# Performance work log

Hardware: AMD Instinct MI355X
Metric: run time of the kernel (lower is better)

Reference implementation:

```python
import jax, jax.numpy as jnp
import numpy as np

NUM_ROUTING_ITER = 3

def _squash(x):
    # Faithful to torch x.norm(): GLOBAL Frobenius norm over the whole tensor.
    n2 = jnp.sum(x * x)
    return x * (jnp.sqrt(n2) / (1.0 + n2))

def setup_inputs() -> dict:
    key = jax.random.key(0)
    k1, k2 = jax.random.split(key)
    x = jax.random.normal(k1, (256, 1152, 8), dtype=jnp.float32)
    weight = jax.random.normal(k2, (10, 1152, 8, 16), dtype=jnp.float32)
    return {"x": x, "weight": weight}

def reference(x, weight):
    # priors: [NC, B, IC, 1, OC] from [1,B,IC,1,L] @ [NC,1,IC,L,OC]
    priors = jnp.einsum('bil,nilo->nbio', x, weight)[:, :, :, None, :]
    b = jnp.zeros_like(priors)
    v = None
    for _ in range(NUM_ROUTING_ITER):
        # legacy F.softmax with no dim on a 5D tensor -> dim=1 (batch dim)
        c = jax.nn.softmax(b, axis=1)
        s = jnp.sum(c * priors, axis=2, keepdims=True)  # [NC,B,1,1,OC]
        v = _squash(s)
        b = b + jnp.sum(priors * v, axis=-1, keepdims=True)
    return v
```

## Files before the change

### kernel.cpp

```cpp
#include <hip/hip_runtime.h>
#include <math.h>

#define NC    10
#define BATCH 256
#define IC    1152
#define LDIM  8
#define OC    16

#define NCH   96
#define CH    (IC/NCH)
#define NBLK  (NC*NCH)
#define NTHR  256
#define NTOT  (NC*BATCH*OC)
#define NRED  (NTOT/NTHR)

typedef float f32x2 __attribute__((ext_vector_type(2)));

__device__ __forceinline__ int xcd_swizzle(int bid, int nwg) {
    int cpx = nwg >> 3;
    return (bid & 7) * cpx + (bid >> 3);
}

__global__ __launch_bounds__(256) void k0_xT(const float* __restrict__ x,
                                             float* __restrict__ xT)
{
    int u = blockIdx.x * 256 + threadIdx.x;
    int i = u >> 9, r = u & 511, b = r >> 1, h = r & 1;
    reinterpret_cast<float4*>(xT)[u] =
        reinterpret_cast<const float4*>(x)[((size_t)b * IC + i) * 2 + h];
}

__global__ __launch_bounds__(256) void kA(
    const float* __restrict__ xT, const float* __restrict__ w,
    float* __restrict__ s_part)
{
    int wg = xcd_swizzle(blockIdx.x, NBLK);
    int n  = wg / NCH, ch = wg % NCH;
    int i0 = ch * CH;
    int t  = threadIdx.x;

    f32x2 sp2[8];
#pragma unroll
    for (int j = 0; j < 8; ++j) sp2[j] = (f32x2){0.f, 0.f};

    for (int ii = 0; ii < CH; ++ii) {
        int i = i0 + ii;
        const float4* xp = reinterpret_cast<const float4*>(xT)
                         + ((size_t)i * BATCH + t) * 2;
        float4 xa = xp[0], xb = xp[1];
        float xr[8] = {xa.x, xa.y, xa.z, xa.w, xb.x, xb.y, xb.z, xb.w};
        const f32x2* wp2 = reinterpret_cast<const f32x2*>(
            w + (size_t)__builtin_amdgcn_readfirstlane((n * IC + i) * (LDIM * OC)));
#pragma unroll
        for (int l = 0; l < LDIM; ++l) {
            f32x2 xl = {xr[l], xr[l]};
#pragma unroll
            for (int j = 0; j < 8; ++j)
                sp2[j] += wp2[l * 8 + j] * xl;
        }
    }
    float4* dst = reinterpret_cast<float4*>(s_part)
                + (((size_t)ch * NC + n) * BATCH + t) * 4;
    const float inv = 1.0f / 256.0f;
    dst[0] = make_float4(sp2[0].x*inv, sp2[0].y*inv, sp2[1].x*inv, sp2[1].y*inv);
    dst[1] = make_float4(sp2[2].x*inv, sp2[2].y*inv, sp2[3].x*inv, sp2[3].y*inv);
    dst[2] = make_float4(sp2[4].x*inv, sp2[4].y*inv, sp2[5].x*inv, sp2[5].y*inv);
    dst[3] = make_float4(sp2[6].x*inv, sp2[6].y*inv, sp2[7].x*inv, sp2[7].y*inv);
}

__global__ __launch_bounds__(256) void kR(const float* __restrict__ s_part,
                                          float* __restrict__ s,
                                          float* __restrict__ n2_part)
{
    int idx = blockIdx.x * 256 + threadIdx.x;
    float acc = 0.f;
    for (int c2 = 0; c2 < NCH; ++c2) acc += s_part[(size_t)c2 * NTOT + idx];
    s[idx] = acc;
    float q = acc * acc;
#pragma unroll
    for (int m = 32; m >= 1; m >>= 1) q += __shfl_xor(q, m, 64);
    __shared__ float r[4];
    int lane = threadIdx.x & 63, wid = threadIdx.x >> 6;
    if (lane == 0) r[wid] = q;
    __syncthreads();
    if (threadIdx.x == 0) n2_part[blockIdx.x] = r[0] + r[1] + r[2] + r[3];
}

template<bool FIRST>
__global__ __launch_bounds__(256) void kB(
    const float* __restrict__ xT, const float* __restrict__ w,
    const float* __restrict__ s, const float* __restrict__ n2_part,
    float* __restrict__ betaT, float* __restrict__ s_part)
{
    __shared__ float redA[2][4];
    __shared__ float redW[4];
    int t = threadIdx.x, lane = t & 63, wid = t >> 6;
    int wg = xcd_swizzle(blockIdx.x, NBLK);
    int n  = wg / NCH, ch = wg % NCH;
    int i0 = ch * CH;

    float q = (t < NRED) ? n2_part[t] : 0.f;
#pragma unroll
    for (int m = 32; m >= 1; m >>= 1) q += __shfl_xor(q, m, 64);
    if (lane == 0) redW[wid] = q;
    __syncthreads();
    float n2 = redW[0] + redW[1] + redW[2] + redW[3];
    float sc = sqrtf(n2) / (1.0f + n2);

    f32x2 v2[8];
    {
        const f32x2* svp = reinterpret_cast<const f32x2*>(s)
                         + ((size_t)n * BATCH + t) * 8;
        f32x2 scv = {sc, sc};
#pragma unroll
        for (int j = 0; j < 8; ++j) v2[j] = svp[j] * scv;
    }

    f32x2 sp2[8];
#pragma unroll
    for (int j = 0; j < 8; ++j) sp2[j] = (f32x2){0.f, 0.f};

    for (int ii = 0; ii < CH; ++ii) {
        int i = i0 + ii;
        const float4* xp = reinterpret_cast<const float4*>(xT)
                         + ((size_t)i * BATCH + t) * 2;
        float4 xa = xp[0], xb = xp[1];
        float xr[8] = {xa.x, xa.y, xa.z, xa.w, xb.x, xb.y, xb.z, xb.w};
        const f32x2* wp2 = reinterpret_cast<const f32x2*>(
            w + (size_t)__builtin_amdgcn_readfirstlane((n * IC + i) * (LDIM * OC)));

        f32x2 p2[8];
#pragma unroll
        for (int j = 0; j < 8; ++j) p2[j] = (f32x2){0.f, 0.f};
#pragma unroll
        for (int l = 0; l < LDIM; ++l) {
            f32x2 xl = {xr[l], xr[l]};
#pragma unroll
            for (int j = 0; j < 8; ++j)
                p2[j] += wp2[l * 8 + j] * xl;
        }

        f32x2 d2 = p2[0] * v2[0];
#pragma unroll
        for (int j = 1; j < 8; ++j) d2 += p2[j] * v2[j];
        float dot = d2.x + d2.y;

        size_t bidx = ((size_t)n * IC + i) * BATCH + t;
        float beta;
        if (FIRST) { beta = dot; betaT[bidx] = beta; }
        else       { beta = betaT[bidx] + dot; }

        float e = __expf(beta);
        float es = e;
#pragma unroll
        for (int m = 1; m < 64; m <<= 1) es += __shfl_xor(es, m, 64);
        if (lane == 0) redA[ii & 1][wid] = es;
        __syncthreads();
        float denom = redA[ii & 1][0] + redA[ii & 1][1]
                    + redA[ii & 1][2] + redA[ii & 1][3];
        float c = e * (1.0f / denom);
        f32x2 c2 = {c, c};
#pragma unroll
        for (int j = 0; j < 8; ++j) sp2[j] += c2 * p2[j];
    }

    float4* dst = reinterpret_cast<float4*>(s_part)
                + (((size_t)ch * NC + n) * BATCH + t) * 4;
    dst[0] = make_float4(sp2[0].x, sp2[0].y, sp2[1].x, sp2[1].y);
    dst[1] = make_float4(sp2[2].x, sp2[2].y, sp2[3].x, sp2[3].y);
    dst[2] = make_float4(sp2[4].x, sp2[4].y, sp2[5].x, sp2[5].y);
    dst[3] = make_float4(sp2[6].x, sp2[6].y, sp2[7].x, sp2[7].y);
}

__global__ __launch_bounds__(256) void k_out(const float* __restrict__ s,
                                             const float* __restrict__ n2_part,
                                             float* __restrict__ out)
{
    int t = threadIdx.x, lane = t & 63, wid = t >> 6;
    float q = (t < NRED) ? n2_part[t] : 0.f;
#pragma unroll
    for (int m = 32; m >= 1; m >>= 1) q += __shfl_xor(q, m, 64);
    __shared__ float r[4];
    if (lane == 0) r[wid] = q;
    __syncthreads();
    float n2 = r[0] + r[1] + r[2] + r[3];
    float sc = sqrtf(n2) / (1.0f + n2);
    int idx = blockIdx.x * 256 + t;
    out[idx] = s[idx] * sc;
}

extern "C" void kernel_launch(void* const* d_in, const int* in_sizes, int n_in,
                              void* d_out, int out_size, void* d_ws, size_t ws_size,
                              hipStream_t stream)
{
    const float* x = (const float*)d_in[0];
    const float* w = (const float*)d_in[1];
    float* out = (float*)d_out;
    float* ws  = (float*)d_ws;

    float* xT      = ws;
    float* betaT   = xT + (size_t)IC * BATCH * LDIM;
    float* s       = betaT + (size_t)NC * IC * BATCH;
    float* s_part  = s + (size_t)NC * BATCH * OC;
    float* n2_part = s_part + (size_t)NCH * NC * BATCH * OC;

    dim3 blk(256);

    k0_xT<<<2304, blk, 0, stream>>>(x, xT);
    kA<<<NBLK, blk, 0, stream>>>(xT, w, s_part);
    kR<<<NRED, blk, 0, stream>>>(s_part, s, n2_part);
    kB<true><<<NBLK, blk, 0, stream>>>(xT, w, s, n2_part, betaT, s_part);
    kR<<<NRED, blk, 0, stream>>>(s_part, s, n2_part);
    kB<false><<<NBLK, blk, 0, stream>>>(xT, w, s, n2_part, betaT, s_part);
    kR<<<NRED, blk, 0, stream>>>(s_part, s, n2_part);
    k_out<<<NRED, blk, 0, stream>>>(s, n2_part, out);
}
```

Before: 98.27 us.

## Double chunk count, split reduction across waves, and prefetch x in routing kernel

Doubles the number of input-capsule chunks so kA and kB launch twice as many workgroups, each handling fewer capsules. The partial-sum reduction kernel now splits the chunk loop across four waves per block with an LDS combine, producing 640 norm partials that a shared helper reduces. kB also software-prefetches the next capsule's x values to hide load latency behind the per-capsule barrier. In exchange, the partial-sum buffer doubles in size and the reduce reads more data.

```diff
diff --git a/kernel.cpp b/kernel.cpp
--- a/kernel.cpp
+++ b/kernel.cpp
@@ -7,18 +7,31 @@
 #define LDIM  8
 #define OC    16
 
-#define NCH   96
+#define NCH   192
 #define CH    (IC/NCH)
 #define NBLK  (NC*NCH)
 #define NTHR  256
 #define NTOT  (NC*BATCH*OC)
-#define NRED  (NTOT/NTHR)
+#define NRB   (NTOT/64)
+#define KPG   (NCH/4)
 
 typedef float f32x2 __attribute__((ext_vector_type(2)));
 
 __device__ __forceinline__ int xcd_swizzle(int bid, int nwg) {
     int cpx = nwg >> 3;
     return (bid & 7) * cpx + (bid >> 3);
+}
+
+__device__ __forceinline__ float n2_reduce(const float* __restrict__ n2_part,
+                                           float* redW, int t, int lane, int wid)
+{
+    float q = n2_part[t] + n2_part[t + 256];
+    if (t < 128) q += n2_part[t + 512];
+#pragma unroll
+    for (int m = 32; m >= 1; m >>= 1) q += __shfl_xor(q, m, 64);
+    if (lane == 0) redW[wid] = q;
+    __syncthreads();
+    return redW[0] + redW[1] + redW[2] + redW[3];
 }
 
 __global__ __launch_bounds__(256) void k0_xT(const float* __restrict__ x,
@@ -72,18 +85,22 @@
                                           float* __restrict__ s,
                                           float* __restrict__ n2_part)
 {
-    int idx = blockIdx.x * 256 + threadIdx.x;
+    __shared__ float lds[4][64];
+    int t = threadIdx.x, lane = t & 63, g = t >> 6;
+    int idx0 = blockIdx.x * 64;
     float acc = 0.f;
-    for (int c2 = 0; c2 < NCH; ++c2) acc += s_part[(size_t)c2 * NTOT + idx];
-    s[idx] = acc;
-    float q = acc * acc;
-#pragma unroll
-    for (int m = 32; m >= 1; m >>= 1) q += __shfl_xor(q, m, 64);
-    __shared__ float r[4];
-    int lane = threadIdx.x & 63, wid = threadIdx.x >> 6;
-    if (lane == 0) r[wid] = q;
+    for (int k = 0; k < KPG; ++k)
+        acc += s_part[(size_t)(g * KPG + k) * NTOT + idx0 + lane];
+    lds[g][lane] = acc;
     __syncthreads();
-    if (threadIdx.x == 0) n2_part[blockIdx.x] = r[0] + r[1] + r[2] + r[3];
+    if (t < 64) {
+        float sv = lds[0][t] + lds[1][t] + lds[2][t] + lds[3][t];
+        s[idx0 + t] = sv;
+        float q = sv * sv;
+#pragma unroll
+        for (int m = 32; m >= 1; m >>= 1) q += __shfl_xor(q, m, 64);
+        if (t == 0) n2_part[blockIdx.x] = q;
+    }
 }
 
 template<bool FIRST>
@@ -99,12 +116,7 @@
     int n  = wg / NCH, ch = wg % NCH;
     int i0 = ch * CH;
 
-    float q = (t < NRED) ? n2_part[t] : 0.f;
-#pragma unroll
-    for (int m = 32; m >= 1; m >>= 1) q += __shfl_xor(q, m, 64);
-    if (lane == 0) redW[wid] = q;
-    __syncthreads();
-    float n2 = redW[0] + redW[1] + redW[2] + redW[3];
+    float n2 = n2_reduce(n2_part, redW, t, lane, wid);
     float sc = sqrtf(n2) / (1.0f + n2);
 
     f32x2 v2[8];
@@ -120,11 +132,18 @@
 #pragma unroll
     for (int j = 0; j < 8; ++j) sp2[j] = (f32x2){0.f, 0.f};
 
+    const float4* xbase = reinterpret_cast<const float4*>(xT);
+    size_t xo = ((size_t)i0 * BATCH + t) * 2;
+    float4 xa = xbase[xo], xb = xbase[xo + 1];
+
     for (int ii = 0; ii < CH; ++ii) {
         int i = i0 + ii;
-        const float4* xp = reinterpret_cast<const float4*>(xT)
-                         + ((size_t)i * BATCH + t) * 2;
-        float4 xa = xp[0], xb = xp[1];
+        float4 na = xa, nb = xb;
+        if (ii + 1 < CH) {
+            size_t nx = ((size_t)(i + 1) * BATCH + t) * 2;
+            na = xbase[nx]; nb = xbase[nx + 1];
+        }
+
         float xr[8] = {xa.x, xa.y, xa.z, xa.w, xb.x, xb.y, xb.z, xb.w};
         const f32x2* wp2 = reinterpret_cast<const f32x2*>(
             w + (size_t)__builtin_amdgcn_readfirstlane((n * IC + i) * (LDIM * OC)));
@@ -162,6 +181,8 @@
         f32x2 c2 = {c, c};
 #pragma unroll
         for (int j = 0; j < 8; ++j) sp2[j] += c2 * p2[j];
+
+        xa = na; xb = nb;
     }
 
     float4* dst = reinterpret_cast<float4*>(s_part)
@@ -176,14 +197,9 @@
                                              const float* __restrict__ n2_part,
                                              float* __restrict__ out)
 {
+    __shared__ float redW[4];
     int t = threadIdx.x, lane = t & 63, wid = t >> 6;
-    float q = (t < NRED) ? n2_part[t] : 0.f;
-#pragma unroll
-    for (int m = 32; m >= 1; m >>= 1) q += __shfl_xor(q, m, 64);
-    __shared__ float r[4];
-    if (lane == 0) r[wid] = q;
-    __syncthreads();
-    float n2 = r[0] + r[1] + r[2] + r[3];
+    float n2 = n2_reduce(n2_part, redW, t, lane, wid);
     float sc = sqrtf(n2) / (1.0f + n2);
     int idx = blockIdx.x * 256 + t;
     out[idx] = s[idx] * sc;
@@ -208,10 +224,10 @@
 
     k0_xT<<<2304, blk, 0, stream>>>(x, xT);
     kA<<<NBLK, blk, 0, stream>>>(xT, w, s_part);
-    kR<<<NRED, blk, 0, stream>>>(s_part, s, n2_part);
+    kR<<<NRB, blk, 0, stream>>>(s_part, s, n2_part);
     kB<true><<<NBLK, blk, 0, stream>>>(xT, w, s, n2_part, betaT, s_part);
-    kR<<<NRED, blk, 0, stream>>>(s_part, s, n2_part);
+    kR<<<NRB, blk, 0, stream>>>(s_part, s, n2_part);
     kB<false><<<NBLK, blk, 0, stream>>>(xT, w, s, n2_part, betaT, s_part);
-    kR<<<NRED, blk, 0, stream>>>(s_part, s, n2_part);
-    k_out<<<NRED, blk, 0, stream>>>(s, n2_part, out);
-}
+    kR<<<NRB, blk, 0, stream>>>(s_part, s, n2_part);
+    k_out<<<160, blk, 0, stream>>>(s, n2_part, out);
+}
```

Measured after the change: 144.0 us. +46.6%, slower.

## Drop stored routing logits by summing squashed vectors, split softmax into two passes

Applied to the files above, without the earlier changes.

The routing logits are no longer written to and read back from a global beta buffer. Because b accumulates dot(priors, v_k), the second iteration instead dots priors with v1+v2 directly, keeping s1 and s2 in separate buffers. Each kB now runs two passes: the first computes exp values into LDS along with per-wave partial sums, then one barrier, and the second recomputes the priors and accumulates c*p. This replaces a barrier per input capsule with a single barrier, at the cost of recomputing the prior matmul and using more LDS. The reduction kernel is also reworked into 160 blocks, each reading float4 across four groups of chunk slices and combining them through LDS.

```diff
diff --git a/kernel.cpp b/kernel.cpp
--- a/kernel.cpp
+++ b/kernel.cpp
@@ -12,7 +12,8 @@
 #define NBLK  (NC*NCH)
 #define NTHR  256
 #define NTOT  (NC*BATCH*OC)
-#define NRED  (NTOT/NTHR)
+#define NRED  160
+#define KPG   (NCH/4)
 
 typedef float f32x2 __attribute__((ext_vector_type(2)));
 
@@ -72,53 +73,81 @@
                                           float* __restrict__ s,
                                           float* __restrict__ n2_part)
 {
-    int idx = blockIdx.x * 256 + threadIdx.x;
-    float acc = 0.f;
-    for (int c2 = 0; c2 < NCH; ++c2) acc += s_part[(size_t)c2 * NTOT + idx];
-    s[idx] = acc;
-    float q = acc * acc;
-#pragma unroll
-    for (int m = 32; m >= 1; m >>= 1) q += __shfl_xor(q, m, 64);
-    __shared__ float r[4];
-    int lane = threadIdx.x & 63, wid = threadIdx.x >> 6;
-    if (lane == 0) r[wid] = q;
-    __syncthreads();
-    if (threadIdx.x == 0) n2_part[blockIdx.x] = r[0] + r[1] + r[2] + r[3];
-}
-
-template<bool FIRST>
+    __shared__ float4 lds[4][64];
+    int t = threadIdx.x, lane = t & 63, g = t >> 6;
+    int idx0 = blockIdx.x * 256;
+    const float* base = s_part + idx0 + lane * 4;
+    float4 a0 = make_float4(0,0,0,0), a1 = a0, a2 = a0, a3 = a0;
+    for (int k = 0; k < KPG; k += 4) {
+        float4 v0 = *reinterpret_cast<const float4*>(base + (size_t)(g*KPG + k    ) * NTOT);
+        float4 v1 = *reinterpret_cast<const float4*>(base + (size_t)(g*KPG + k + 1) * NTOT);
+        float4 v2 = *reinterpret_cast<const float4*>(base + (size_t)(g*KPG + k + 2) * NTOT);
+        float4 v3 = *reinterpret_cast<const float4*>(base + (size_t)(g*KPG + k + 3) * NTOT);
+        a0.x += v0.x; a0.y += v0.y; a0.z += v0.z; a0.w += v0.w;
+        a1.x += v1.x; a1.y += v1.y; a1.z += v1.z; a1.w += v1.w;
+        a2.x += v2.x; a2.y += v2.y; a2.z += v2.z; a2.w += v2.w;
+        a3.x += v3.x; a3.y += v3.y; a3.z += v3.z; a3.w += v3.w;
+    }
+    float4 a = make_float4((a0.x+a1.x)+(a2.x+a3.x), (a0.y+a1.y)+(a2.y+a3.y),
+                           (a0.z+a1.z)+(a2.z+a3.z), (a0.w+a1.w)+(a2.w+a3.w));
+    lds[g][lane] = a;
+    __syncthreads();
+    if (t < 64) {
+        float4 s0 = lds[0][t], s1 = lds[1][t], s2 = lds[2][t], s3 = lds[3][t];
+        float4 sv = make_float4((s0.x+s1.x)+(s2.x+s3.x), (s0.y+s1.y)+(s2.y+s3.y),
+                                (s0.z+s1.z)+(s2.z+s3.z), (s0.w+s1.w)+(s2.w+s3.w));
+        *reinterpret_cast<float4*>(s + idx0 + t * 4) = sv;
+        float q = sv.x*sv.x + sv.y*sv.y + sv.z*sv.z + sv.w*sv.w;
+#pragma unroll
+        for (int m = 32; m >= 1; m >>= 1) q += __shfl_xor(q, m, 64);
+        if (t == 0) n2_part[blockIdx.x] = q;
+    }
+}
+
+template<int MODE>
 __global__ __launch_bounds__(256) void kB(
     const float* __restrict__ xT, const float* __restrict__ w,
-    const float* __restrict__ s, const float* __restrict__ n2_part,
-    float* __restrict__ betaT, float* __restrict__ s_part)
-{
-    __shared__ float redA[2][4];
-    __shared__ float redW[4];
+    const float* __restrict__ s1, const float* __restrict__ n2p1,
+    const float* __restrict__ s2, const float* __restrict__ n2p2,
+    float* __restrict__ s_part)
+{
+    __shared__ float e_lds[CH][NTHR];
+    __shared__ float esW[CH][4];
+    __shared__ float redW[8];
     int t = threadIdx.x, lane = t & 63, wid = t >> 6;
     int wg = xcd_swizzle(blockIdx.x, NBLK);
     int n  = wg / NCH, ch = wg % NCH;
     int i0 = ch * CH;
 
-    float q = (t < NRED) ? n2_part[t] : 0.f;
-#pragma unroll
-    for (int m = 32; m >= 1; m >>= 1) q += __shfl_xor(q, m, 64);
-    if (lane == 0) redW[wid] = q;
-    __syncthreads();
-    float n2 = redW[0] + redW[1] + redW[2] + redW[3];
-    float sc = sqrtf(n2) / (1.0f + n2);
+    float q1 = (t < NRED) ? n2p1[t] : 0.f;
+    float q2 = (MODE == 2 && t < NRED) ? n2p2[t] : 0.f;
+#pragma unroll
+    for (int m = 32; m >= 1; m >>= 1) {
+        q1 += __shfl_xor(q1, m, 64);
+        if (MODE == 2) q2 += __shfl_xor(q2, m, 64);
+    }
+    if (lane == 0) { redW[wid] = q1; redW[4 + wid] = q2; }
+    __syncthreads();
+    float n2a = (redW[0] + redW[1]) + (redW[2] + redW[3]);
+    float sc1 = sqrtf(n2a) / (1.0f + n2a);
 
     f32x2 v2[8];
     {
-        const f32x2* svp = reinterpret_cast<const f32x2*>(s)
+        const f32x2* s1p = reinterpret_cast<const f32x2*>(s1)
                          + ((size_t)n * BATCH + t) * 8;
-        f32x2 scv = {sc, sc};
-#pragma unroll
-        for (int j = 0; j < 8; ++j) v2[j] = svp[j] * scv;
-    }
-
-    f32x2 sp2[8];
-#pragma unroll
-    for (int j = 0; j < 8; ++j) sp2[j] = (f32x2){0.f, 0.f};
+        f32x2 sv = {sc1, sc1};
+#pragma unroll
+        for (int j = 0; j < 8; ++j) v2[j] = s1p[j] * sv;
+        if (MODE == 2) {
+            float n2b = (redW[4] + redW[5]) + (redW[6] + redW[7]);
+            float sc2 = sqrtf(n2b) / (1.0f + n2b);
+            const f32x2* s2p = reinterpret_cast<const f32x2*>(s2)
+                             + ((size_t)n * BATCH + t) * 8;
+            f32x2 sw = {sc2, sc2};
+#pragma unroll
+            for (int j = 0; j < 8; ++j) v2[j] += s2p[j] * sw;
+        }
+    }
 
     for (int ii = 0; ii < CH; ++ii) {
         int i = i0 + ii;
@@ -128,7 +157,6 @@
         float xr[8] = {xa.x, xa.y, xa.z, xa.w, xb.x, xb.y, xb.z, xb.w};
         const f32x2* wp2 = reinterpret_cast<const f32x2*>(
             w + (size_t)__builtin_amdgcn_readfirstlane((n * IC + i) * (LDIM * OC)));
-
         f32x2 p2[8];
 #pragma unroll
         for (int j = 0; j < 8; ++j) p2[j] = (f32x2){0.f, 0.f};
@@ -139,26 +167,42 @@
             for (int j = 0; j < 8; ++j)
                 p2[j] += wp2[l * 8 + j] * xl;
         }
-
         f32x2 d2 = p2[0] * v2[0];
 #pragma unroll
         for (int j = 1; j < 8; ++j) d2 += p2[j] * v2[j];
-        float dot = d2.x + d2.y;
-
-        size_t bidx = ((size_t)n * IC + i) * BATCH + t;
-        float beta;
-        if (FIRST) { beta = dot; betaT[bidx] = beta; }
-        else       { beta = betaT[bidx] + dot; }
-
-        float e = __expf(beta);
+        float e = __expf(d2.x + d2.y);
+        e_lds[ii][t] = e;
         float es = e;
 #pragma unroll
         for (int m = 1; m < 64; m <<= 1) es += __shfl_xor(es, m, 64);
-        if (lane == 0) redA[ii & 1][wid] = es;
-        __syncthreads();
-        float denom = redA[ii & 1][0] + redA[ii & 1][1]
-                    + redA[ii & 1][2] + redA[ii & 1][3];
-        float c = e * (1.0f / denom);
+        if (lane == 0) esW[ii][wid] = es;
+    }
+    __syncthreads();
+
+    f32x2 sp2[8];
+#pragma unroll
+    for (int j = 0; j < 8; ++j) sp2[j] = (f32x2){0.f, 0.f};
+
+    for (int ii = 0; ii < CH; ++ii) {
+        int i = i0 + ii;
+        const float4* xp = reinterpret_cast<const float4*>(xT)
+                         + ((size_t)i * BATCH + t) * 2;
+        float4 xa = xp[0], xb = xp[1];
+        float xr[8] = {xa.x, xa.y, xa.z, xa.w, xb.x, xb.y, xb.z, xb.w};
+        const f32x2* wp2 = reinterpret_cast<const f32x2*>(
+            w + (size_t)__builtin_amdgcn_readfirstlane((n * IC + i) * (LDIM * OC)));
+        f32x2 p2[8];
+#pragma unroll
+        for (int j = 0; j < 8; ++j) p2[j] = (f32x2){0.f, 0.f};
+#pragma unroll
+        for (int l = 0; l < LDIM; ++l) {
+            f32x2 xl = {xr[l], xr[l]};
+#pragma unroll
+            for (int j = 0; j < 8; ++j)
+                p2[j] += wp2[l * 8 + j] * xl;
+        }
+        float denom = (esW[ii][0] + esW[ii][1]) + (esW[ii][2] + esW[ii][3]);
+        float c = e_lds[ii][t] * (1.0f / denom);
         f32x2 c2 = {c, c};
 #pragma unroll
         for (int j = 0; j < 8; ++j) sp2[j] += c2 * p2[j];
@@ -176,14 +220,14 @@
                                              const float* __restrict__ n2_part,
                                              float* __restrict__ out)
 {
+    __shared__ float redW[4];
     int t = threadIdx.x, lane = t & 63, wid = t >> 6;
     float q = (t < NRED) ? n2_part[t] : 0.f;
 #pragma unroll
     for (int m = 32; m >= 1; m >>= 1) q += __shfl_xor(q, m, 64);
-    __shared__ float r[4];
-    if (lane == 0) r[wid] = q;
-    __syncthreads();
-    float n2 = r[0] + r[1] + r[2] + r[3];
+    if (lane == 0) redW[wid] = q;
+    __syncthreads();
+    float n2 = (redW[0] + redW[1]) + (redW[2] + redW[3]);
     float sc = sqrtf(n2) / (1.0f + n2);
     int idx = blockIdx.x * 256 + t;
     out[idx] = s[idx] * sc;
@@ -199,19 +243,22 @@
     float* ws  = (float*)d_ws;
 
     float* xT      = ws;
-    float* betaT   = xT + (size_t)IC * BATCH * LDIM;
-    float* s       = betaT + (size_t)NC * IC * BATCH;
-    float* s_part  = s + (size_t)NC * BATCH * OC;
-    float* n2_part = s_part + (size_t)NCH * NC * BATCH * OC;
+    float* s_part  = xT + (size_t)IC * BATCH * LDIM;
+    float* s1      = s_part + (size_t)NCH * NTOT;
+    float* s2      = s1 + NTOT;
+    float* s3      = s2 + NTOT;
+    float* n2p1    = s3 + NTOT;
+    float* n2p2    = n2p1 + NRED;
+    float* n2p3    = n2p2 + NRED;
 
     dim3 blk(256);
 
     k0_xT<<<2304, blk, 0, stream>>>(x, xT);
     kA<<<NBLK, blk, 0, stream>>>(xT, w, s_part);
-    kR<<<NRED, blk, 0, stream>>>(s_part, s, n2_part);
-    kB<true><<<NBLK, blk, 0, stream>>>(xT, w, s, n2_part, betaT, s_part);
-    kR<<<NRED, blk, 0, stream>>>(s_part, s, n2_part);
-    kB<false><<<NBLK, blk, 0, stream>>>(xT, w, s, n2_part, betaT, s_part);
-    kR<<<NRED, blk, 0, stream>>>(s_part, s, n2_part);
-    k_out<<<NRED, blk, 0, stream>>>(s, n2_part, out);
-}
+    kR<<<NRED, blk, 0, stream>>>(s_part, s1, n2p1);
+    kB<1><<<NBLK, blk, 0, stream>>>(xT, w, s1, n2p1, s1, n2p1, s_part);
+    kR<<<NRED, blk, 0, stream>>>(s_part, s2, n2p2);
+    kB<2><<<NBLK, blk, 0, stream>>>(xT, w, s1, n2p1, s2, n2p2, s_part);
+    kR<<<NRED, blk, 0, stream>>>(s_part, s3, n2p3);
+    k_out<<<NRED, blk, 0, stream>>>(s3, n2p3, out);
+}
```

Result: slower. 114.5 us (+16.5%).
